# Kernel optimization log

Measured on AMD Instinct MI355X. Metric: run time of the kernel, lower is better.

Reference implementation:

```python
import jax, jax.numpy as jnp
import numpy as np

B, HH, WW, E = 8, 64, 64, 384
NH, EXP = 6, 2
D1 = (EXP * E) // NH * NH      # 768
HD = D1 // NH                  # 128
RPE = 512
LAYERS = 3
EPS = 1e-6


def srms(x):
    # SimpleRMSNorm: no learnable weight
    return x * jax.lax.rsqrt(jnp.mean(x * x, axis=-1, keepdims=True) + EPS)


def rpe_forward(pos, pw, pb, lw, lb, ow, ob):
    # pos: (n, 1) -> (n, NH*HD). Rpe MLP: act(pos_proj) -> layers x [norm,act,linear] -> out
    x = jax.nn.relu(pos @ pw + pb)
    for i in range(lw.shape[0]):  # fixed small layer count
        x = jax.nn.relu(srms(x)) @ lw[i] + lb[i]
    return jax.nn.relu(srms(x)) @ ow + ob


def tno_coeffs(n, pw, pb, lw, lb, ow, ob):
    # Toeplitz coeffs t_0..t_{n-1}, t_0(dummy), t_{-(n-1)}..t_{-1} for circular conv of len 2n
    pos = jnp.arange(1, n, dtype=jnp.float32)[:, None]             # (n-1, 1), par_type=1
    neg = -jnp.arange(1, n, dtype=jnp.float32)[::-1][:, None]      # -(n-1)..-1
    zero = jnp.zeros((1, 1), dtype=jnp.float32)
    t_zero = rpe_forward(zero, pw, pb, lw, lb, ow, ob)             # (1, NH*HD)
    t_pos = rpe_forward(pos, pw, pb, lw, lb, ow, ob)               # (n-1, NH*HD)
    t_neg = rpe_forward(neg, pw, pb, lw, lb, ow, ob)
    a = jnp.concatenate([t_zero, t_pos, t_zero, t_neg], axis=0)    # (2n, NH*HD)
    return a.reshape(2 * n, NH, HD).transpose(1, 0, 2)             # (NH, 2n, HD)


def tno_apply(v, a, axis):
    # v: (b, h, H, W, d); FFT-based Toeplitz (circular) mixing along `axis` in {-3, -2}
    n = v.shape[axis]
    a = a[:, :, None, :] if axis == -3 else a[:, None, :, :]
    y = jnp.fft.rfft(v, 2 * n, axis=axis)
    af = jnp.fft.rfft(a, 2 * n, axis=axis)
    out = jnp.fft.irfft(af * y, 2 * n, axis=axis)
    return jax.lax.slice_in_dim(out, 0, n, axis=out.ndim + axis)


def setup_inputs() -> dict:
    key = jax.random.key(0)
    ks = jax.random.split(key, 24)
    s = 0.02
    def rn(k, shape):
        return jax.random.normal(k, shape, dtype=jnp.float32) * s
    inp = {
        "x": jax.random.normal(ks[0], (B, HH, WW, E), dtype=jnp.float32),
        "H": HH, "W": WW,
        "Wu": rn(ks[1], (E, D1)), "bu": jnp.zeros((D1,), jnp.float32),
        "Wv": rn(ks[2], (E, D1)), "bv": jnp.zeros((D1,), jnp.float32),
        "Wo": rn(ks[3], (D1, E)), "bo": jnp.zeros((E,), jnp.float32),
    }
    for t, off in (("r1", 4), ("r2", 10)):
        inp[t + "_pw"] = rn(ks[off], (1, RPE))
        inp[t + "_pb"] = jnp.zeros((RPE,), jnp.float32)
        inp[t + "_lw"] = rn(ks[off + 1], (LAYERS, RPE, RPE))
        inp[t + "_lb"] = jnp.zeros((LAYERS, RPE), jnp.float32)
        inp[t + "_ow"] = rn(ks[off + 2], (RPE, NH * HD))
        inp[t + "_ob"] = jnp.zeros((NH * HD,), jnp.float32)
    return inp


def reference(x, H, W, Wu, bu, Wv, bv, Wo, bo,
              r1_pw, r1_pb, r1_lw, r1_lb, r1_ow, r1_ob,
              r2_pw, r2_pb, r2_lw, r2_lb, r2_ow, r2_ob):
    b = x.shape[0]
    xn = srms(x)                                    # pre_norm (SimpleRMSNorm)
    u = jax.nn.silu(xn @ Wu + bu)                   # gate branch
    v = jax.nn.silu(xn @ Wv + bv)
    v = v.reshape(b, H, W, NH, HD).transpose(0, 3, 1, 2, 4)        # b h H W d
    a_h = tno_coeffs(H, r2_pw, r2_pb, r2_lw, r2_lb, r2_ow, r2_ob)  # toep2, dim=-3
    a_w = tno_coeffs(W, r1_pw, r1_pb, r1_lw, r1_lb, r1_ow, r1_ob)  # toep1, dim=-2
    out = tno_apply(v, a_h, -3) + tno_apply(v, a_w, -2)
    out = out.transpose(0, 2, 3, 1, 4).reshape(b, H, W, NH * HD)   # b H W (h d)
    out = u * out
    return out @ Wo + bo + x
```

## Files before the change

### kernel.cpp

```cpp
#include <hip/hip_runtime.h>
#include <stdint.h>


typedef __attribute__((ext_vector_type(4))) float  f32x4;
typedef __attribute__((ext_vector_type(8))) short  s16x8;
typedef __attribute__((ext_vector_type(8))) unsigned short u16x8;
typedef __attribute__((ext_vector_type(4))) unsigned short u16x4;
typedef unsigned short u16;

#define M_TOT 32768
#define E_DIM 384
#define D1    768
#define NHEAD 6
#define HDIM  128

__device__ __forceinline__ u16 f2bf(float f) {
  union { float f; unsigned int u; } v; v.f = f;
  unsigned int r = (v.u + 0x7FFFu + ((v.u >> 16) & 1u)) >> 16;
  return (u16)r;
}
__device__ __forceinline__ float bf2f(u16 h) {
  union { unsigned int u; float f; } v; v.u = ((unsigned int)h) << 16;
  return v.f;
}
__device__ __forceinline__ float silu_f(float x) {
  return x * __builtin_amdgcn_rcpf(1.f + __expf(-x));
}

__device__ __forceinline__ void gload_lds16(const u16* g, u16* l) {
  __builtin_amdgcn_global_load_lds(
      (const __attribute__((address_space(1))) uint32_t*)g,
      (__attribute__((address_space(3))) uint32_t*)l, 16, 0, 0);
}

__global__ __launch_bounds__(256) void prep_k(const float* __restrict__ Wu,
                                              const float* __restrict__ Wv,
                                              const float* __restrict__ Wo,
                                              u16* __restrict__ Wuvt,
                                              u16* __restrict__ Wot) {
  int idx = blockIdx.x * 256 + threadIdx.x;
  const int NUV = 1536 * 384;
  if (idx < NUV) {
    int n = idx / 384, k = idx % 384;
    float val = (n < 768) ? Wu[(size_t)k * 768 + n] : Wv[(size_t)k * 768 + (n - 768)];
    Wuvt[idx] = f2bf(val);
  } else {
    int j = idx - NUV;
    if (j < 384 * 768) {
      int n = j / 768, k = j % 768;
      Wot[j] = f2bf(Wo[(size_t)k * 384 + n]);
    }
  }
}

__global__ __launch_bounds__(256) void rpet_k(const float* __restrict__ r1lw,
                                              const float* __restrict__ r1ow,
                                              const float* __restrict__ r2lw,
                                              const float* __restrict__ r2ow,
                                              u16* __restrict__ lwT,
                                              u16* __restrict__ owT) {
  __shared__ float sm[32][33];
  int b = blockIdx.x;
  int mlp = b / 1152;
  int r = b % 1152;
  const float* src;
  u16* dst;
  int C, ty, tx;
  if (r < 768) {
    int L = r / 256, t = r % 256;
    ty = t / 16; tx = t % 16;
    src = (mlp ? r2lw : r1lw) + (size_t)L * 262144;
    dst = lwT + (size_t)(mlp * 3 + L) * 262144;
    C = 512;
  } else {
    int t = r - 768;
    ty = t / 24; tx = t % 24;
    src = mlp ? r2ow : r1ow;
    dst = owT + (size_t)mlp * 393216;
    C = 768;
  }
  int lx = threadIdx.x % 32, ly = threadIdx.x / 32;
#pragma unroll
  for (int q = 0; q < 4; q++) {
    int y = q * 8 + ly;
    sm[y][lx] = src[(size_t)(ty * 32 + y) * C + tx * 32 + lx];
  }
  __syncthreads();
#pragma unroll
  for (int q = 0; q < 4; q++) {
    int y = q * 8 + ly;
    dst[(size_t)(tx * 32 + y) * 512 + ty * 32 + lx] = f2bf(sm[lx][y]);
  }
}

__global__ __launch_bounds__(256) void rms_k(const float* __restrict__ x,
                                             u16* __restrict__ xn) {
  int row  = blockIdx.x * 4 + (threadIdx.x >> 6);
  int lane = threadIdx.x & 63;
  const float* xr = x + (size_t)row * 384 + lane;
  float v[6]; float ss = 0.f;
#pragma unroll
  for (int i = 0; i < 6; i++) { v[i] = xr[i * 64]; ss += v[i] * v[i]; }
#pragma unroll
  for (int off = 32; off > 0; off >>= 1) ss += __shfl_xor(ss, off);
  float sc = rsqrtf(ss * (1.f / 384.f) + 1e-6f);
  u16* o = xn + (size_t)row * 384 + lane;
#pragma unroll
  for (int i = 0; i < 6; i++) o[i * 64] = f2bf(v[i] * sc);
}

__global__ __launch_bounds__(256) void rpe_in_k(const float* __restrict__ r1pw,
                                                const float* __restrict__ r1pb,
                                                const float* __restrict__ r2pw,
                                                const float* __restrict__ r2pb,
                                                float* __restrict__ X0) {
  int idx = blockIdx.x * 256 + threadIdx.x;
  int gid = idx * 4;
  int row = gid >> 9, col = gid & 511;
  int mlp = row >> 7, p = row & 127;
  float pos = (p < 64) ? (float)p : ((p == 64) ? 0.f : (float)(p - 128));
  const float* pw = (mlp ? r2pw : r1pw) + col;
  const float* pb = (mlp ? r2pb : r1pb) + col;
  f32x4 w = *(const f32x4*)pw;
  f32x4 bb = *(const f32x4*)pb;
  f32x4 o;
#pragma unroll
  for (int e = 0; e < 4; e++) o[e] = fmaxf(pos * w[e] + bb[e], 0.f);
  *(f32x4*)(X0 + gid) = o;
}

template <int N>
__global__ __launch_bounds__(256) void rpe_layer_k(
    const float* __restrict__ X,
    const u16* __restrict__ wtA, const u16* __restrict__ wtB,
    const float* __restrict__ bA, const float* __restrict__ bB,
    float* __restrict__ outA, float* __restrict__ outB) {
  constexpr int NT = N / 128;
  const int mlp = blockIdx.x / NT;
  const int n0  = (blockIdx.x % NT) * 128;
  const u16* WT = mlp ? wtB : wtA;
  const float* bias = mlp ? bB : bA;
  float* out = mlp ? outB : outA;
  const float* Xm = X + (size_t)mlp * 128 * 512;

  __shared__ float scale[128];
  __shared__ __align__(16) u16 As[128 * 64];
  __shared__ __align__(16) u16 Bs[128 * 64];

  const int tid  = threadIdx.x;
  const int lane = tid & 63;
  const int wid  = tid >> 6;
  const int wm   = wid >> 1, wn = wid & 1;
  const int fl   = lane & 15, fh = lane >> 4;

  {
    int row = tid >> 1, half = tid & 1;
    const float* xr = Xm + (size_t)row * 512 + half * 256;
    float ss = 0.f;
#pragma unroll 8
    for (int q = 0; q < 64; q++) {
      f32x4 v = *(const f32x4*)(xr + q * 4);
      ss += v[0] * v[0] + v[1] * v[1] + v[2] * v[2] + v[3] * v[3];
    }
    ss += __shfl_xor(ss, 1);
    if (!half) scale[row] = rsqrtf(ss * (1.f / 512.f) + 1e-6f);
  }
  __syncthreads();

  f32x4 acc[4][4];
  {
    f32x4 z = {0.f, 0.f, 0.f, 0.f};
#pragma unroll
    for (int i = 0; i < 4; i++)
#pragma unroll
      for (int j = 0; j < 4; j++) acc[i][j] = z;
  }

  const int arow = tid >> 1, acb = (tid & 1) * 32;
  const int sr = tid >> 3, sc = (tid & 7) * 8;

  for (int kt = 0; kt < 512; kt += 64) {
    {
      const float* xp = Xm + (size_t)arow * 512 + kt + acb;
      float s_ = scale[arow];
      u16* dst = As + arow * 64 + acb;
#pragma unroll
      for (int q = 0; q < 8; q++) {
        f32x4 v = *(const f32x4*)(xp + q * 4);
        u16x4 pk;
#pragma unroll
        for (int e = 0; e < 4; e++) pk[e] = f2bf(fmaxf(v[e], 0.f) * s_);
        *(u16x4*)(dst + q * 4) = pk;
      }
    }
    {
      const u16* gB = WT + (size_t)(n0 + sr) * 512 + kt + sc;
      u16* lB = Bs + sr * 64 + sc;
#pragma unroll
      for (int i = 0; i < 4; i++)
        gload_lds16(gB + (size_t)(i * 32) * 512, lB + i * 32 * 64);
    }
    __syncthreads();
#pragma unroll
    for (int ks = 0; ks < 2; ks++) {
      s16x8 af[4], bfr[4];
      const u16* ap = As + (wm * 64 + fl) * 64 + ks * 32 + fh * 8;
      const u16* bp = Bs + (wn * 64 + fl) * 64 + ks * 32 + fh * 8;
#pragma unroll
      for (int i = 0; i < 4; i++) af[i] = *(const s16x8*)(ap + i * 16 * 64);
#pragma unroll
      for (int j = 0; j < 4; j++) bfr[j] = *(const s16x8*)(bp + j * 16 * 64);
#pragma unroll
      for (int i = 0; i < 4; i++)
#pragma unroll
        for (int j = 0; j < 4; j++)
          acc[i][j] = __builtin_amdgcn_mfma_f32_16x16x32_bf16(af[i], bfr[j], acc[i][j], 0, 0, 0);
    }
    __syncthreads();
  }

#pragma unroll
  for (int i = 0; i < 4; i++)
#pragma unroll
    for (int j = 0; j < 4; j++) {
      int c = n0 + wn * 64 + j * 16 + fl;
      float bv_ = bias[c];
#pragma unroll
      for (int q = 0; q < 4; q++) {
        int r = wm * 64 + i * 16 + fh * 4 + q;
        out[(size_t)r * N + c] = acc[i][j][q] + bv_;
      }
    }
}

template <int MODE>
__global__ __launch_bounds__(256) void gemm_k(
    const u16* __restrict__ A, const u16* __restrict__ Bt, int K,
    u16* __restrict__ u_out, u16* __restrict__ vt_out,
    const float* __restrict__ bu, const float* __restrict__ bv,
    float* __restrict__ out, const float* __restrict__ bo,
    const float* __restrict__ xres) {
  __shared__ __align__(16) char smem[34816];
  u16*   As  = (u16*)smem;
  u16*   Bs  = As + 128 * 64;
  float* epi = (float*)smem;

  const int tid  = threadIdx.x;
  const int lane = tid & 63;
  const int wid  = tid >> 6;
  const int wm   = wid >> 1, wn = wid & 1;
  const int bm   = blockIdx.x & 255, bn = blockIdx.x >> 8;
  const int m0   = bm * 128, n0 = bn * 128;
  const int fl   = lane & 15, fh = lane >> 4;

  f32x4 acc[4][4];
  {
    f32x4 z = {0.f, 0.f, 0.f, 0.f};
#pragma unroll
    for (int i = 0; i < 4; i++)
#pragma unroll
      for (int j = 0; j < 4; j++) acc[i][j] = z;
  }

  const int sr  = tid >> 3;
  const int scl = (tid & 7) * 8;
  const int scs = ((tid & 7) ^ (sr & 7)) * 8;

  for (int kt = 0; kt < K; kt += 64) {
    const u16* gA = A  + (size_t)(m0 + sr) * K + kt + scs;
    const u16* gB = Bt + (size_t)(n0 + sr) * K + kt + scs;
    u16* lA = As + sr * 64 + scl;
    u16* lB = Bs + sr * 64 + scl;
#pragma unroll
    for (int i = 0; i < 4; i++) {
      gload_lds16(gA + (size_t)(i * 32) * K, lA + i * 32 * 64);
      gload_lds16(gB + (size_t)(i * 32) * K, lB + i * 32 * 64);
    }
    __syncthreads();
#pragma unroll
    for (int ks = 0; ks < 2; ks++) {
      s16x8 af[4], bfr[4];
      const int xc = ((ks * 4 + fh) ^ (fl & 7)) * 8;
      const u16* ap = As + (wm * 64 + fl) * 64 + xc;
      const u16* bp = Bs + (wn * 64 + fl) * 64 + xc;
#pragma unroll
      for (int i = 0; i < 4; i++) af[i] = *(const s16x8*)(ap + i * 16 * 64);
#pragma unroll
      for (int j = 0; j < 4; j++) bfr[j] = *(const s16x8*)(bp + j * 16 * 64);
#pragma unroll
      for (int i = 0; i < 4; i++)
#pragma unroll
        for (int j = 0; j < 4; j++)
          acc[i][j] = __builtin_amdgcn_mfma_f32_16x16x32_bf16(af[i], bfr[j], acc[i][j], 0, 0, 0);
    }
    __syncthreads();
  }

  for (int half = 0; half < 2; half++) {
    __syncthreads();
    if (wm == half) {
#pragma unroll
      for (int i = 0; i < 4; i++)
#pragma unroll
        for (int j = 0; j < 4; j++) {
          int er = i * 16 + fh * 4;
          int ec = wn * 64 + j * 16 + fl;
#pragma unroll
          for (int q = 0; q < 4; q++) epi[(er + q) * 132 + ec] = acc[i][j][q];
        }
    }
    __syncthreads();
    if (MODE == 0) {
      if (n0 < 768) {
        int rr = tid >> 2;
        int gm = m0 + half * 64 + rr;
        u16* dst = u_out + (size_t)gm * 768 + n0;
#pragma unroll
        for (int q = 0; q < 4; q++) {
          int cb = (tid & 3) * 8 + q * 32;
          u16x8 pk;
#pragma unroll
          for (int e = 0; e < 8; e++) {
            int c = cb + e;
            pk[e] = f2bf(silu_f(epi[rr * 132 + c] + bu[n0 + c]));
          }
          *(u16x8*)(dst + cb) = pk;
        }
      } else {
        int cc = tid >> 1;
        int cg = n0 - 768 + cc;
        float bias = bv[cg];
        u16* dst = vt_out + (size_t)cg * M_TOT + m0 + half * 64;
#pragma unroll
        for (int q = 0; q < 4; q++) {
          int mb = (tid & 1) * 8 + q * 16;
          u16x8 pk;
#pragma unroll
          for (int e = 0; e < 8; e++) {
            int mm = mb + e;
            pk[e] = f2bf(silu_f(epi[mm * 132 + cc] + bias));
          }
          *(u16x8*)(dst + mb) = pk;
        }
      }
    } else {
      int rr = tid >> 2;
      int gm = m0 + half * 64 + rr;
      const float* xr = xres + (size_t)gm * 384 + n0;
      float* orow = out + (size_t)gm * 384 + n0;
#pragma unroll
      for (int q = 0; q < 8; q++) {
        int cb = (tid & 3) * 4 + q * 16;
        f32x4 xv = *(const f32x4*)(xr + cb);
        f32x4 ov;
#pragma unroll
        for (int e = 0; e < 4; e++) {
          int c = cb + e;
          ov[e] = epi[rr * 132 + c] + bo[n0 + c] + xv[e];
        }
        *(f32x4*)(orow + cb) = ov;
      }
    }
  }
}

__global__ __launch_bounds__(256) void conv_k(const u16* __restrict__ vt,
                                              const float* __restrict__ a_h,
                                              const float* __restrict__ a_w,
                                              u16* __restrict__ cst) {
  __shared__ __align__(16) char smraw[4 * 64 * 72 * 2 + 1024];
  u16* Vs  = (u16*)smraw;
  u16* VTs = Vs + 64 * 72;
  u16* Ths = VTs + 64 * 72;
  u16* Tws = Ths + 64 * 72;
  float* ahs = (float*)(Tws + 64 * 72);
  float* aws = ahs + 128;
  u16* epi = Ths;

  const int tid = threadIdx.x;
  const int c = blockIdx.x >> 3, b = blockIdx.x & 7;
  const u16* src = vt + (size_t)c * M_TOT + b * 4096;

  {
    int y = tid >> 2, x0 = (tid & 3) * 16;
    u16x8 p0 = *(const u16x8*)(src + y * 64 + x0);
    u16x8 p1 = *(const u16x8*)(src + y * 64 + x0 + 8);
    *(u16x8*)(Vs + y * 72 + x0) = p0;
    *(u16x8*)(Vs + y * 72 + x0 + 8) = p1;
  }
  if (tid < 128) ahs[tid] = a_h[(size_t)tid * 768 + c];
  else           aws[tid - 128] = a_w[(size_t)(tid - 128) * 768 + c];
  __syncthreads();

  {
    int y = tid & 63, j0 = (tid >> 6) * 16;
#pragma unroll
    for (int e = 0; e < 16; e++) {
      int j = j0 + e;
      VTs[j * 72 + y] = Vs[y * 72 + j];
      Ths[y * 72 + j] = f2bf(ahs[(y - j) & 127]);
      Tws[y * 72 + j] = f2bf(aws[(y - j) & 127]);
    }
  }
  __syncthreads();

  const int lane = tid & 63, w = tid >> 6;
  const int fl = lane & 15, fh = lane >> 4;
  f32x4 acc[4];
  {
    f32x4 z = {0.f, 0.f, 0.f, 0.f};
#pragma unroll
    for (int i = 0; i < 4; i++) acc[i] = z;
  }

#pragma unroll
  for (int ks = 0; ks < 2; ks++) {
    s16x8 qh = *(const s16x8*)(Ths + (w * 16 + fl) * 72 + ks * 32 + fh * 8);
#pragma unroll
    for (int i = 0; i < 4; i++) {
      s16x8 p = *(const s16x8*)(VTs + (i * 16 + fl) * 72 + ks * 32 + fh * 8);
      acc[i] = __builtin_amdgcn_mfma_f32_16x16x32_bf16(p, qh, acc[i], 0, 0, 0);
    }
    s16x8 qw = *(const s16x8*)(Vs + (w * 16 + fl) * 72 + ks * 32 + fh * 8);
#pragma unroll
    for (int i = 0; i < 4; i++) {
      s16x8 p = *(const s16x8*)(Tws + (i * 16 + fl) * 72 + ks * 32 + fh * 8);
      acc[i] = __builtin_amdgcn_mfma_f32_16x16x32_bf16(p, qw, acc[i], 0, 0, 0);
    }
  }
  __syncthreads();

#pragma unroll
  for (int i = 0; i < 4; i++) {
    u16x4 pk;
#pragma unroll
    for (int e = 0; e < 4; e++) pk[e] = f2bf(acc[i][e]);
    *(u16x4*)(epi + (w * 16 + fl) * 72 + i * 16 + fh * 4) = pk;
  }
  __syncthreads();

  {
    int y = tid >> 2, x0 = (tid & 3) * 16;
    u16x8 a0 = *(const u16x8*)(epi + y * 72 + x0);
    u16x8 a1 = *(const u16x8*)(epi + y * 72 + x0 + 8);
    u16* dst = cst + (size_t)c * M_TOT + b * 4096 + y * 64 + x0;
    *(u16x8*)dst = a0;
    *(u16x8*)(dst + 8) = a1;
  }
}

__global__ __launch_bounds__(256) void transmul_k(const u16* __restrict__ cst,
                                                  const u16* __restrict__ u,
                                                  u16* __restrict__ g) {
  __shared__ u16 ct[64 * 72];
  const int tid = threadIdx.x;
  int bm = blockIdx.x / 12, bc = blockIdx.x % 12;
  int m0 = bm * 64, c0 = bc * 64;
  {
    int cc = tid >> 2, sg = (tid & 3) * 8;
    const u16* src = cst + (size_t)(c0 + cc) * M_TOT + m0 + sg;
    *(u16x8*)(ct + cc * 72 + sg)      = *(const u16x8*)(src);
    *(u16x8*)(ct + cc * 72 + sg + 32) = *(const u16x8*)(src + 32);
  }
  __syncthreads();
  int mr = tid >> 2;
  int gm = m0 + mr;
  const u16* up = u + (size_t)gm * 768 + c0;
  u16* gp = g + (size_t)gm * 768 + c0;
#pragma unroll
  for (int q = 0; q < 2; q++) {
    int cb = (tid & 3) * 8 + q * 32;
    u16x8 uv = *(const u16x8*)(up + cb);
    u16x8 pk;
#pragma unroll
    for (int e = 0; e < 8; e++) {
      int c = cb + e;
      pk[e] = f2bf(bf2f(uv[e]) * bf2f(ct[c * 72 + mr]));
    }
    *(u16x8*)(gp + cb) = pk;
  }
}

extern "C" void kernel_launch(void* const* d_in, const int* in_sizes, int n_in,
                              void* d_out, int out_size, void* d_ws, size_t ws_size,
                              hipStream_t stream) {
  const float* x    = (const float*)d_in[0];
  const float* Wu   = (const float*)d_in[3];
  const float* bu   = (const float*)d_in[4];
  const float* Wv   = (const float*)d_in[5];
  const float* bv   = (const float*)d_in[6];
  const float* Wo   = (const float*)d_in[7];
  const float* bo   = (const float*)d_in[8];
  const float* r1pw = (const float*)d_in[9];
  const float* r1pb = (const float*)d_in[10];
  const float* r1lw = (const float*)d_in[11];
  const float* r1lb = (const float*)d_in[12];
  const float* r1ow = (const float*)d_in[13];
  const float* r1ob = (const float*)d_in[14];
  const float* r2pw = (const float*)d_in[15];
  const float* r2pb = (const float*)d_in[16];
  const float* r2lw = (const float*)d_in[17];
  const float* r2lb = (const float*)d_in[18];
  const float* r2ow = (const float*)d_in[19];
  const float* r2ob = (const float*)d_in[20];
  float* outp = (float*)d_out;

  char* ws = (char*)d_ws;
  size_t off = 0;
  auto carve = [&](size_t bytes) {
    char* p = ws + off;
    off += (bytes + 255) & ~(size_t)255;
    return p;
  };
  u16*   xn   = (u16*)carve((size_t)M_TOT * 384 * 2);
  u16*   u    = (u16*)carve((size_t)M_TOT * 768 * 2);
  u16*   vt   = (u16*)carve((size_t)768 * M_TOT * 2);
  u16*   cst  = (u16*)carve((size_t)768 * M_TOT * 2);
  u16*   Wuvt = (u16*)carve((size_t)1536 * 384 * 2);
  u16*   Wot  = (u16*)carve((size_t)384 * 768 * 2);
  float* aw_t = (float*)carve((size_t)128 * 768 * 4);
  float* ah_t = (float*)carve((size_t)128 * 768 * 4);
  u16*   g    = vt;

  char* rb  = (char*)cst;
  u16*   lwT = (u16*)rb;
  u16*   owT = (u16*)(rb + 3145728);
  float* X0  = (float*)(rb + 3145728 + 1572864);
  float* X1  = X0 + 256 * 512;

  prep_k<<<3456, 256, 0, stream>>>(Wu, Wv, Wo, Wuvt, Wot);
  rpet_k<<<2304, 256, 0, stream>>>(r1lw, r1ow, r2lw, r2ow, lwT, owT);
  rms_k<<<8192, 256, 0, stream>>>(x, xn);

  rpe_in_k<<<128, 256, 0, stream>>>(r1pw, r1pb, r2pw, r2pb, X0);
  rpe_layer_k<512><<<8, 256, 0, stream>>>(X0, lwT, lwT + 3 * 262144,
                                          r1lb, r2lb, X1, X1 + 128 * 512);
  rpe_layer_k<512><<<8, 256, 0, stream>>>(X1, lwT + 262144, lwT + 4 * 262144,
                                          r1lb + 512, r2lb + 512, X0, X0 + 128 * 512);
  rpe_layer_k<512><<<8, 256, 0, stream>>>(X0, lwT + 2 * 262144, lwT + 5 * 262144,
                                          r1lb + 1024, r2lb + 1024, X1, X1 + 128 * 512);
  rpe_layer_k<768><<<12, 256, 0, stream>>>(X1, owT, owT + 393216,
                                           r1ob, r2ob, aw_t, ah_t);

  gemm_k<0><<<256 * 12, 256, 0, stream>>>(xn, Wuvt, 384,
                                          u, vt, bu, bv,
                                          nullptr, nullptr, nullptr);
  conv_k<<<768 * 8, 256, 0, stream>>>(vt, ah_t, aw_t, cst);
  transmul_k<<<512 * 12, 256, 0, stream>>>(cst, u, g);
  gemm_k<1><<<256 * 3, 256, 0, stream>>>(g, Wot, 768,
                                         nullptr, nullptr, nullptr, nullptr,
                                         outp, bo, x);
}
```

Measured before the change: 445.6 us.

## Fuse gating into conv kernel, store u transposed, merge setup kernels

The first GEMM now writes u in channel-major layout like v. The conv kernel loads u tiles and multiplies the gate in its epilogue, which removes the separate transmul pass and the cst round trip. The final GEMM reads the channel-major gated activations and transposes them into LDS with per-element stores instead of async global-to-LDS loads. The weight prep, RPE transpose, RMS norm and RPE input kernels are merged into a single launch, and the RPE output coefficients are written transposed for contiguous loads. The risk is that the scattered LDS transpose stores in the last GEMM cost more than the transmul pass they replace.

New measurement: 432.4 us. 1.03x faster.

```diff
diff --git a/kernel.cpp b/kernel.cpp
--- a/kernel.cpp
+++ b/kernel.cpp
@@ -11,8 +11,6 @@
 #define M_TOT 32768
 #define E_DIM 384
 #define D1    768
-#define NHEAD 6
-#define HDIM  128
 
 __device__ __forceinline__ u16 f2bf(float f) {
   union { float f; unsigned int u; } v; v.f = f;
@@ -33,103 +31,90 @@
       (__attribute__((address_space(3))) uint32_t*)l, 16, 0, 0);
 }
 
-__global__ __launch_bounds__(256) void prep_k(const float* __restrict__ Wu,
-                                              const float* __restrict__ Wv,
-                                              const float* __restrict__ Wo,
-                                              u16* __restrict__ Wuvt,
-                                              u16* __restrict__ Wot) {
-  int idx = blockIdx.x * 256 + threadIdx.x;
-  const int NUV = 1536 * 384;
-  if (idx < NUV) {
-    int n = idx / 384, k = idx % 384;
-    float val = (n < 768) ? Wu[(size_t)k * 768 + n] : Wv[(size_t)k * 768 + (n - 768)];
-    Wuvt[idx] = f2bf(val);
+__global__ __launch_bounds__(256) void setup_k(
+    const float* __restrict__ x, u16* __restrict__ xn,
+    const float* __restrict__ Wu, const float* __restrict__ Wv,
+    const float* __restrict__ Wo, u16* __restrict__ Wuvt, u16* __restrict__ Wot,
+    const float* __restrict__ r1lw, const float* __restrict__ r1ow,
+    const float* __restrict__ r2lw, const float* __restrict__ r2ow,
+    u16* __restrict__ lwT, u16* __restrict__ owT,
+    const float* __restrict__ r1pw, const float* __restrict__ r1pb,
+    const float* __restrict__ r2pw, const float* __restrict__ r2pb,
+    float* __restrict__ X0) {
+  __shared__ float sm[32][33];
+  const int bid = blockIdx.x;
+  const int tid = threadIdx.x;
+
+  if (bid < 8192) {
+    int row  = bid * 4 + (tid >> 6);
+    int lane = tid & 63;
+    const float* xr = x + (size_t)row * 384 + lane;
+    float v[6]; float ss = 0.f;
+#pragma unroll
+    for (int i = 0; i < 6; i++) { v[i] = xr[i * 64]; ss += v[i] * v[i]; }
+#pragma unroll
+    for (int off = 32; off > 0; off >>= 1) ss += __shfl_xor(ss, off);
+    float sc = rsqrtf(ss * (1.f / 384.f) + 1e-6f);
+    u16* o = xn + (size_t)row * 384 + lane;
+#pragma unroll
+    for (int i = 0; i < 6; i++) o[i * 64] = f2bf(v[i] * sc);
+  } else if (bid < 11360) {
+    int b = bid - 8192;
+    const float* src; u16* dst; int C, DS, R0, C0;
+    if (b < 2304) {
+      int mlp = b / 1152, r = b % 1152;
+      if (r < 768) {
+        int L = r / 256, t = r % 256;
+        R0 = (t / 16) * 32; C0 = (t % 16) * 32;
+        src = (mlp ? r2lw : r1lw) + (size_t)L * 262144;
+        dst = lwT + (size_t)(mlp * 3 + L) * 262144;
+        C = 512; DS = 512;
+      } else {
+        int t = r - 768;
+        R0 = (t / 24) * 32; C0 = (t % 24) * 32;
+        src = mlp ? r2ow : r1ow;
+        dst = owT + (size_t)mlp * 393216;
+        C = 768; DS = 512;
+      }
+    } else {
+      int t = b - 2304;
+      if (t < 288)      { R0 = (t / 24) * 32; C0 = (t % 24) * 32;
+                          src = Wu; C = 768; dst = Wuvt;            DS = 384; }
+      else if (t < 576) { int t2 = t - 288; R0 = (t2 / 24) * 32; C0 = (t2 % 24) * 32;
+                          src = Wv; C = 768; dst = Wuvt + 768 * 384; DS = 384; }
+      else              { int t2 = t - 576; R0 = (t2 / 12) * 32; C0 = (t2 % 12) * 32;
+                          src = Wo; C = 384; dst = Wot;             DS = 768; }
+    }
+    int lx = tid % 32, ly = tid / 32;
+#pragma unroll
+    for (int q = 0; q < 4; q++) {
+      int y = q * 8 + ly;
+      sm[y][lx] = src[(size_t)(R0 + y) * C + C0 + lx];
+    }
+    __syncthreads();
+#pragma unroll
+    for (int q = 0; q < 4; q++) {
+      int y = q * 8 + ly;
+      dst[(size_t)(C0 + y) * DS + R0 + lx] = f2bf(sm[lx][y]);
+    }
   } else {
-    int j = idx - NUV;
-    if (j < 384 * 768) {
-      int n = j / 768, k = j % 768;
-      Wot[j] = f2bf(Wo[(size_t)k * 384 + n]);
-    }
-  }
-}
-
-__global__ __launch_bounds__(256) void rpet_k(const float* __restrict__ r1lw,
-                                              const float* __restrict__ r1ow,
-                                              const float* __restrict__ r2lw,
-                                              const float* __restrict__ r2ow,
-                                              u16* __restrict__ lwT,
-                                              u16* __restrict__ owT) {
-  __shared__ float sm[32][33];
-  int b = blockIdx.x;
-  int mlp = b / 1152;
-  int r = b % 1152;
-  const float* src;
-  u16* dst;
-  int C, ty, tx;
-  if (r < 768) {
-    int L = r / 256, t = r % 256;
-    ty = t / 16; tx = t % 16;
-    src = (mlp ? r2lw : r1lw) + (size_t)L * 262144;
-    dst = lwT + (size_t)(mlp * 3 + L) * 262144;
-    C = 512;
-  } else {
-    int t = r - 768;
-    ty = t / 24; tx = t % 24;
-    src = mlp ? r2ow : r1ow;
-    dst = owT + (size_t)mlp * 393216;
-    C = 768;
-  }
-  int lx = threadIdx.x % 32, ly = threadIdx.x / 32;
-#pragma unroll
-  for (int q = 0; q < 4; q++) {
-    int y = q * 8 + ly;
-    sm[y][lx] = src[(size_t)(ty * 32 + y) * C + tx * 32 + lx];
-  }
-  __syncthreads();
-#pragma unroll
-  for (int q = 0; q < 4; q++) {
-    int y = q * 8 + ly;
-    dst[(size_t)(tx * 32 + y) * 512 + ty * 32 + lx] = f2bf(sm[lx][y]);
-  }
-}
-
-__global__ __launch_bounds__(256) void rms_k(const float* __restrict__ x,
-                                             u16* __restrict__ xn) {
-  int row  = blockIdx.x * 4 + (threadIdx.x >> 6);
-  int lane = threadIdx.x & 63;
-  const float* xr = x + (size_t)row * 384 + lane;
-  float v[6]; float ss = 0.f;
-#pragma unroll
-  for (int i = 0; i < 6; i++) { v[i] = xr[i * 64]; ss += v[i] * v[i]; }
-#pragma unroll
-  for (int off = 32; off > 0; off >>= 1) ss += __shfl_xor(ss, off);
-  float sc = rsqrtf(ss * (1.f / 384.f) + 1e-6f);
-  u16* o = xn + (size_t)row * 384 + lane;
-#pragma unroll
-  for (int i = 0; i < 6; i++) o[i * 64] = f2bf(v[i] * sc);
-}
-
-__global__ __launch_bounds__(256) void rpe_in_k(const float* __restrict__ r1pw,
-                                                const float* __restrict__ r1pb,
-                                                const float* __restrict__ r2pw,
-                                                const float* __restrict__ r2pb,
-                                                float* __restrict__ X0) {
-  int idx = blockIdx.x * 256 + threadIdx.x;
-  int gid = idx * 4;
-  int row = gid >> 9, col = gid & 511;
-  int mlp = row >> 7, p = row & 127;
-  float pos = (p < 64) ? (float)p : ((p == 64) ? 0.f : (float)(p - 128));
-  const float* pw = (mlp ? r2pw : r1pw) + col;
-  const float* pb = (mlp ? r2pb : r1pb) + col;
-  f32x4 w = *(const f32x4*)pw;
-  f32x4 bb = *(const f32x4*)pb;
-  f32x4 o;
-#pragma unroll
-  for (int e = 0; e < 4; e++) o[e] = fmaxf(pos * w[e] + bb[e], 0.f);
-  *(f32x4*)(X0 + gid) = o;
-}
-
-template <int N>
+    int idx = (bid - 11360) * 256 + tid;
+    int gid = idx * 4;
+    int row = gid >> 9, col = gid & 511;
+    int mlp = row >> 7, p = row & 127;
+    float pos = (p < 64) ? (float)p : ((p == 64) ? 0.f : (float)(p - 128));
+    const float* pw = (mlp ? r2pw : r1pw) + col;
+    const float* pb = (mlp ? r2pb : r1pb) + col;
+    f32x4 w = *(const f32x4*)pw;
+    f32x4 bb = *(const f32x4*)pb;
+    f32x4 o;
+#pragma unroll
+    for (int e = 0; e < 4; e++) o[e] = fmaxf(pos * w[e] + bb[e], 0.f);
+    *(f32x4*)(X0 + gid) = o;
+  }
+}
+
+template <int N, bool TOUT>
 __global__ __launch_bounds__(256) void rpe_layer_k(
     const float* __restrict__ X,
     const u16* __restrict__ wtA, const u16* __restrict__ wtB,
@@ -228,7 +213,8 @@
 #pragma unroll
       for (int q = 0; q < 4; q++) {
         int r = wm * 64 + i * 16 + fh * 4 + q;
-        out[(size_t)r * N + c] = acc[i][j][q] + bv_;
+        if (TOUT) out[(size_t)c * 128 + r] = acc[i][j][q] + bv_;
+        else      out[(size_t)r * N + c]   = acc[i][j][q] + bv_;
       }
     }
 }
@@ -265,16 +251,36 @@
   const int sr  = tid >> 3;
   const int scl = (tid & 7) * 8;
   const int scs = ((tid & 7) ^ (sr & 7)) * 8;
+  const int cr  = tid & 63;
+  const int mw  = ((tid >> 6) & 3) * 32;
 
   for (int kt = 0; kt < K; kt += 64) {
-    const u16* gA = A  + (size_t)(m0 + sr) * K + kt + scs;
-    const u16* gB = Bt + (size_t)(n0 + sr) * K + kt + scs;
-    u16* lA = As + sr * 64 + scl;
-    u16* lB = Bs + sr * 64 + scl;
-#pragma unroll
-    for (int i = 0; i < 4; i++) {
-      gload_lds16(gA + (size_t)(i * 32) * K, lA + i * 32 * 64);
-      gload_lds16(gB + (size_t)(i * 32) * K, lB + i * 32 * 64);
+    if (MODE == 1) {
+      const u16* ga = A + (size_t)(kt + cr) * M_TOT + m0 + mw;
+      u16x8 rr[4];
+      rr[0] = *(const u16x8*)(ga);
+      rr[1] = *(const u16x8*)(ga + 8);
+      rr[2] = *(const u16x8*)(ga + 16);
+      rr[3] = *(const u16x8*)(ga + 24);
+      const int cb8 = cr >> 3, off = cr & 7;
+#pragma unroll
+      for (int v = 0; v < 4; v++)
+#pragma unroll
+        for (int e = 0; e < 8; e++)
+          As[(mw + v * 8 + e) * 64 + ((cb8 ^ e) << 3) + off] = rr[v][e];
+    } else {
+      const u16* gA = A + (size_t)(m0 + sr) * K + kt + scs;
+      u16* lA = As + sr * 64 + scl;
+#pragma unroll
+      for (int i = 0; i < 4; i++)
+        gload_lds16(gA + (size_t)(i * 32) * K, lA + i * 32 * 64);
+    }
+    {
+      const u16* gB = Bt + (size_t)(n0 + sr) * K + kt + scs;
+      u16* lB = Bs + sr * 64 + scl;
+#pragma unroll
+      for (int i = 0; i < 4; i++)
+        gload_lds16(gB + (size_t)(i * 32) * K, lB + i * 32 * 64);
     }
     __syncthreads();
 #pragma unroll
@@ -311,37 +317,22 @@
     }
     __syncthreads();
     if (MODE == 0) {
-      if (n0 < 768) {
-        int rr = tid >> 2;
-        int gm = m0 + half * 64 + rr;
-        u16* dst = u_out + (size_t)gm * 768 + n0;
-#pragma unroll
-        for (int q = 0; q < 4; q++) {
-          int cb = (tid & 3) * 8 + q * 32;
-          u16x8 pk;
-#pragma unroll
-          for (int e = 0; e < 8; e++) {
-            int c = cb + e;
-            pk[e] = f2bf(silu_f(epi[rr * 132 + c] + bu[n0 + c]));
-          }
-          *(u16x8*)(dst + cb) = pk;
+      const bool isU = (n0 < 768);
+      u16* baseo = isU ? u_out : vt_out;
+      const int cc = tid >> 1;
+      const int cg = (isU ? n0 : n0 - 768) + cc;
+      const float bias_v = (isU ? bu : bv)[cg];
+      u16* dst = baseo + (size_t)cg * M_TOT + m0 + half * 64;
+#pragma unroll
+      for (int q = 0; q < 4; q++) {
+        int mb = (tid & 1) * 8 + q * 16;
+        u16x8 pk;
+#pragma unroll
+        for (int e = 0; e < 8; e++) {
+          int mm = mb + e;
+          pk[e] = f2bf(silu_f(epi[mm * 132 + cc] + bias_v));
         }
-      } else {
-        int cc = tid >> 1;
-        int cg = n0 - 768 + cc;
-        float bias = bv[cg];
-        u16* dst = vt_out + (size_t)cg * M_TOT + m0 + half * 64;
-#pragma unroll
-        for (int q = 0; q < 4; q++) {
-          int mb = (tid & 1) * 8 + q * 16;
-          u16x8 pk;
-#pragma unroll
-          for (int e = 0; e < 8; e++) {
-            int mm = mb + e;
-            pk[e] = f2bf(silu_f(epi[mm * 132 + cc] + bias));
-          }
-          *(u16x8*)(dst + mb) = pk;
-        }
+        *(u16x8*)(dst + mb) = pk;
       }
     } else {
       int rr = tid >> 2;
@@ -365,31 +356,34 @@
 }
 
 __global__ __launch_bounds__(256) void conv_k(const u16* __restrict__ vt,
-                                              const float* __restrict__ a_h,
-                                              const float* __restrict__ a_w,
-                                              u16* __restrict__ cst) {
-  __shared__ __align__(16) char smraw[4 * 64 * 72 * 2 + 1024];
+                                              const u16* __restrict__ ut,
+                                              const float* __restrict__ a_hT,
+                                              const float* __restrict__ a_wT,
+                                              u16* __restrict__ gT) {
+  __shared__ __align__(16) char smraw[5 * 64 * 72 * 2 + 1024];
   u16* Vs  = (u16*)smraw;
   u16* VTs = Vs + 64 * 72;
   u16* Ths = VTs + 64 * 72;
   u16* Tws = Ths + 64 * 72;
-  float* ahs = (float*)(Tws + 64 * 72);
+  u16* Us  = Tws + 64 * 72;
+  float* ahs = (float*)(Us + 64 * 72);
   float* aws = ahs + 128;
   u16* epi = Ths;
 
   const int tid = threadIdx.x;
   const int c = blockIdx.x >> 3, b = blockIdx.x & 7;
-  const u16* src = vt + (size_t)c * M_TOT + b * 4096;
+  const u16* srcv = vt + (size_t)c * M_TOT + b * 4096;
+  const u16* srcu = ut + (size_t)c * M_TOT + b * 4096;
 
   {
     int y = tid >> 2, x0 = (tid & 3) * 16;
-    u16x8 p0 = *(const u16x8*)(src + y * 64 + x0);
-    u16x8 p1 = *(const u16x8*)(src + y * 64 + x0 + 8);
-    *(u16x8*)(Vs + y * 72 + x0) = p0;
-    *(u16x8*)(Vs + y * 72 + x0 + 8) = p1;
-  }
-  if (tid < 128) ahs[tid] = a_h[(size_t)tid * 768 + c];
-  else           aws[tid - 128] = a_w[(size_t)(tid - 128) * 768 + c];
+    *(u16x8*)(Vs + y * 72 + x0)     = *(const u16x8*)(srcv + y * 64 + x0);
+    *(u16x8*)(Vs + y * 72 + x0 + 8) = *(const u16x8*)(srcv + y * 64 + x0 + 8);
+    *(u16x8*)(Us + y * 72 + x0)     = *(const u16x8*)(srcu + y * 64 + x0);
+    *(u16x8*)(Us + y * 72 + x0 + 8) = *(const u16x8*)(srcu + y * 64 + x0 + 8);
+  }
+  if (tid < 128) ahs[tid] = a_hT[(size_t)c * 128 + tid];
+  else           aws[tid - 128] = a_wT[(size_t)c * 128 + (tid - 128)];
   __syncthreads();
 
   {
@@ -430,12 +424,18 @@
   }
   __syncthreads();
 
-#pragma unroll
-  for (int i = 0; i < 4; i++) {
-    u16x4 pk;
-#pragma unroll
-    for (int e = 0; e < 4; e++) pk[e] = f2bf(acc[i][e]);
-    *(u16x4*)(epi + (w * 16 + fl) * 72 + i * 16 + fh * 4) = pk;
+  {
+    int y = w * 16 + fl;
+#pragma unroll
+    for (int i = 0; i < 4; i++) {
+      u16x4 pk;
+#pragma unroll
+      for (int e = 0; e < 4; e++) {
+        int xx = i * 16 + fh * 4 + e;
+        pk[e] = f2bf(acc[i][e] * bf2f(Us[y * 72 + xx]));
+      }
+      *(u16x4*)(epi + y * 72 + i * 16 + fh * 4) = pk;
+    }
   }
   __syncthreads();
 
@@ -443,41 +443,9 @@
     int y = tid >> 2, x0 = (tid & 3) * 16;
     u16x8 a0 = *(const u16x8*)(epi + y * 72 + x0);
     u16x8 a1 = *(const u16x8*)(epi + y * 72 + x0 + 8);
-    u16* dst = cst + (size_t)c * M_TOT + b * 4096 + y * 64 + x0;
+    u16* dst = gT + (size_t)c * M_TOT + b * 4096 + y * 64 + x0;
     *(u16x8*)dst = a0;
     *(u16x8*)(dst + 8) = a1;
-  }
-}
-
-__global__ __launch_bounds__(256) void transmul_k(const u16* __restrict__ cst,
-                                                  const u16* __restrict__ u,
-                                                  u16* __restrict__ g) {
-  __shared__ u16 ct[64 * 72];
-  const int tid = threadIdx.x;
-  int bm = blockIdx.x / 12, bc = blockIdx.x % 12;
-  int m0 = bm * 64, c0 = bc * 64;
-  {
-    int cc = tid >> 2, sg = (tid & 3) * 8;
-    const u16* src = cst + (size_t)(c0 + cc) * M_TOT + m0 + sg;
-    *(u16x8*)(ct + cc * 72 + sg)      = *(const u16x8*)(src);
-    *(u16x8*)(ct + cc * 72 + sg + 32) = *(const u16x8*)(src + 32);
-  }
-  __syncthreads();
-  int mr = tid >> 2;
-  int gm = m0 + mr;
-  const u16* up = u + (size_t)gm * 768 + c0;
-  u16* gp = g + (size_t)gm * 768 + c0;
-#pragma unroll
-  for (int q = 0; q < 2; q++) {
-    int cb = (tid & 3) * 8 + q * 32;
-    u16x8 uv = *(const u16x8*)(up + cb);
-    u16x8 pk;
-#pragma unroll
-    for (int e = 0; e < 8; e++) {
-      int c = cb + e;
-      pk[e] = f2bf(bf2f(uv[e]) * bf2f(ct[c * 72 + mr]));
-    }
-    *(u16x8*)(gp + cb) = pk;
   }
 }
 
@@ -513,41 +481,38 @@
     return p;
   };
   u16*   xn   = (u16*)carve((size_t)M_TOT * 384 * 2);
-  u16*   u    = (u16*)carve((size_t)M_TOT * 768 * 2);
-  u16*   vt   = (u16*)carve((size_t)768 * M_TOT * 2);
-  u16*   cst  = (u16*)carve((size_t)768 * M_TOT * 2);
+  u16*   uT   = (u16*)carve((size_t)768 * M_TOT * 2);
+  u16*   vT   = (u16*)carve((size_t)768 * M_TOT * 2);
+  u16*   gT   = (u16*)carve((size_t)768 * M_TOT * 2);
   u16*   Wuvt = (u16*)carve((size_t)1536 * 384 * 2);
   u16*   Wot  = (u16*)carve((size_t)384 * 768 * 2);
-  float* aw_t = (float*)carve((size_t)128 * 768 * 4);
-  float* ah_t = (float*)carve((size_t)128 * 768 * 4);
-  u16*   g    = vt;
-
-  char* rb  = (char*)cst;
+  float* awT  = (float*)carve((size_t)768 * 128 * 4);
+  float* ahT  = (float*)carve((size_t)768 * 128 * 4);
+
+  char* rb  = (char*)gT;
   u16*   lwT = (u16*)rb;
   u16*   owT = (u16*)(rb + 3145728);
   float* X0  = (float*)(rb + 3145728 + 1572864);
   float* X1  = X0 + 256 * 512;
 
-  prep_k<<<3456, 256, 0, stream>>>(Wu, Wv, Wo, Wuvt, Wot);
-  rpet_k<<<2304, 256, 0, stream>>>(r1lw, r1ow, r2lw, r2ow, lwT, owT);
-  rms_k<<<8192, 256, 0, stream>>>(x, xn);
-
-  rpe_in_k<<<128, 256, 0, stream>>>(r1pw, r1pb, r2pw, r2pb, X0);
-  rpe_layer_k<512><<<8, 256, 0, stream>>>(X0, lwT, lwT + 3 * 262144,
-                                          r1lb, r2lb, X1, X1 + 128 * 512);
-  rpe_layer_k<512><<<8, 256, 0, stream>>>(X1, lwT + 262144, lwT + 4 * 262144,
-                                          r1lb + 512, r2lb + 512, X0, X0 + 128 * 512);
-  rpe_layer_k<512><<<8, 256, 0, stream>>>(X0, lwT + 2 * 262144, lwT + 5 * 262144,
-                                          r1lb + 1024, r2lb + 1024, X1, X1 + 128 * 512);
-  rpe_layer_k<768><<<12, 256, 0, stream>>>(X1, owT, owT + 393216,
-                                           r1ob, r2ob, aw_t, ah_t);
+  setup_k<<<11488, 256, 0, stream>>>(x, xn, Wu, Wv, Wo, Wuvt, Wot,
+                                     r1lw, r1ow, r2lw, r2ow, lwT, owT,
+                                     r1pw, r1pb, r2pw, r2pb, X0);
+
+  rpe_layer_k<512, false><<<8, 256, 0, stream>>>(X0, lwT, lwT + 3 * 262144,
+                                                 r1lb, r2lb, X1, X1 + 128 * 512);
+  rpe_layer_k<512, false><<<8, 256, 0, stream>>>(X1, lwT + 262144, lwT + 4 * 262144,
+                                                 r1lb + 512, r2lb + 512, X0, X0 + 128 * 512);
+  rpe_layer_k<512, false><<<8, 256, 0, stream>>>(X0, lwT + 2 * 262144, lwT + 5 * 262144,
+                                                 r1lb + 1024, r2lb + 1024, X1, X1 + 128 * 512);
+  rpe_layer_k<768, true><<<12, 256, 0, stream>>>(X1, owT, owT + 393216,
+                                                 r1ob, r2ob, awT, ahT);
 
   gemm_k<0><<<256 * 12, 256, 0, stream>>>(xn, Wuvt, 384,
-                                          u, vt, bu, bv,
+                                          uT, vT, bu, bv,
                                           nullptr, nullptr, nullptr);
-  conv_k<<<768 * 8, 256, 0, stream>>>(vt, ah_t, aw_t, cst);
-  transmul_k<<<512 * 12, 256, 0, stream>>>(cst, u, g);
-  gemm_k<1><<<256 * 3, 256, 0, stream>>>(g, Wot, 768,
+  conv_k<<<768 * 8, 256, 0, stream>>>(vT, uT, ahT, awT, gT);
+  gemm_k<1><<<256 * 3, 256, 0, stream>>>(gT, Wot, 768,
                                          nullptr, nullptr, nullptr, nullptr,
                                          outp, bo, x);
 }
```
